# Optimization experiments

Measured on AMD Instinct MI355X. Metric: run time of the kernel, lower is better.

Reference implementation:

```python
import jax, jax.numpy as jnp
import numpy as np

D_MODEL = 192   # embed_dim
DEPTH = 24
D_INNER = 384   # expand=2 * d_model
D_STATE = 16
D_CONV = 4
DT_RANK = 12    # ceil(192/16)
B = 8
IMG = 224
P = 16          # patch size / stride


def setup_inputs() -> dict:
    key = jax.random.key(0)
    ks = jax.random.split(key, 10)
    s = lambda k, shp, sc=0.02: jax.random.normal(k, shp, jnp.float32) * sc
    return {
        "x": jax.random.normal(ks[0], (B, 3, IMG, IMG), jnp.float32),
        "pe_w": s(ks[1], (D_MODEL, 3, P, P)),
        "pe_b": jnp.zeros((D_MODEL,), jnp.float32),
        "norm_w": jnp.ones((DEPTH, D_MODEL), jnp.float32),
        "norm_b": jnp.zeros((DEPTH, D_MODEL), jnp.float32),
        "in_proj_w": s(ks[2], (DEPTH, 2 * D_INNER, D_MODEL)),
        "conv_w": s(ks[3], (DEPTH, D_INNER, D_CONV), 0.1),
        "conv_b": jnp.zeros((DEPTH, D_INNER), jnp.float32),
        "xproj_w": s(ks[4], (DEPTH, DT_RANK + 2 * D_STATE, D_INNER)),
        "dtproj_w": s(ks[5], (DEPTH, D_INNER, DT_RANK), 0.1),
        "dtproj_b": s(ks[6], (DEPTH, D_INNER), 0.1),
        "A_log": jnp.broadcast_to(jnp.log(jnp.arange(1.0, D_STATE + 1.0, dtype=jnp.float32)), (DEPTH, D_INNER, D_STATE)).astype(jnp.float32),
        "D_param": jnp.ones((DEPTH, D_INNER), jnp.float32),
        "outproj_w": s(ks[7], (DEPTH, D_MODEL, D_INNER)),
        "normf_w": jnp.ones((D_MODEL,), jnp.float32),
        "normf_b": jnp.zeros((D_MODEL,), jnp.float32),
    }


def _layernorm(x, w, b, eps=1e-5):
    mu = x.mean(-1, keepdims=True)
    var = ((x - mu) ** 2).mean(-1, keepdims=True)
    return (x - mu) * jax.lax.rsqrt(var + eps) * w + b


def _causal_dwconv(x, w, b):
    # x: [B, L, d_inner]; depthwise causal conv1d (mamba conv1d, padding=d_conv-1, truncated to L)
    xt = jnp.pad(x.swapaxes(1, 2), ((0, 0), (0, 0), (D_CONV - 1, 0)))  # [B, di, L+3]
    y = jax.lax.conv_general_dilated(xt, w[:, None, :], (1,), 'VALID',
                                     feature_group_count=w.shape[0])
    return (y + b[:, None]).swapaxes(1, 2)  # [B, L, di]


def _selective_scan(u, dt, Bm, Cm, A, Dp):
    # u, dt: [B, L, di]; Bm, Cm: [B, L, ds]; A: [di, ds]; Dp: [di]
    dA = jnp.exp(dt[..., None] * A)                         # [B, L, di, ds]
    dBu = (dt * u)[..., None] * Bm[:, :, None, :]           # [B, L, di, ds]

    def step(h, inp):
        dA_t, dBu_t, C_t = inp
        h = dA_t * h + dBu_t                                # [B, di, ds]
        return h, jnp.einsum('bds,bs->bd', h, C_t)

    h0 = jnp.zeros((u.shape[0], A.shape[0], A.shape[1]), u.dtype)
    _, ys = jax.lax.scan(step, h0,
                         (dA.swapaxes(0, 1), dBu.swapaxes(0, 1), Cm.swapaxes(0, 1)))
    return ys.swapaxes(0, 1) + u * Dp                       # [B, L, di]


def _mamba(x, ipw, cw, cb, xpw, dtw, dtb, Alog, Dp, opw):
    xz = jnp.einsum('bld,ed->ble', x, ipw)                  # [B, L, 2*di]
    xin, z = jnp.split(xz, 2, axis=-1)
    xin = jax.nn.silu(_causal_dwconv(xin, cw, cb))
    xdbl = jnp.einsum('bld,ed->ble', xin, xpw)              # [B, L, dt_rank+2*ds]
    dt = jax.nn.softplus(jnp.einsum('blr,dr->bld', xdbl[..., :DT_RANK], dtw) + dtb)
    Bm = xdbl[..., DT_RANK:DT_RANK + D_STATE]
    Cm = xdbl[..., DT_RANK + D_STATE:]
    A = -jnp.exp(Alog)
    y = _selective_scan(xin, dt, Bm, Cm, A, Dp)
    y = y * jax.nn.silu(z)
    return jnp.einsum('bld,ed->ble', y, opw)                # [B, L, D]


def reference(x, pe_w, pe_b, norm_w, norm_b, in_proj_w, conv_w, conv_b,
              xproj_w, dtproj_w, dtproj_b, A_log, D_param, outproj_w,
              normf_w, normf_b):
    # PatchEmbed: conv stride 16 -> flatten -> [B, 196, 192]
    feat = jax.lax.conv_general_dilated(x, pe_w, (P, P), 'VALID') + pe_b[None, :, None, None]
    h = feat.reshape(feat.shape[0], D_MODEL, -1).swapaxes(1, 2)
    residual = None
    for i in range(DEPTH):
        residual = h if residual is None else residual + h
        hn = _layernorm(residual, norm_w[i], norm_b[i])
        h = _mamba(hn, in_proj_w[i], conv_w[i], conv_b[i], xproj_w[i],
                   dtproj_w[i], dtproj_b[i], A_log[i], D_param[i], outproj_w[i])
    residual = residual + h
    return _layernorm(residual, normf_w, normf_b)           # [B, 196, 192]
```

## Files before the change

### kernel.cpp

```cpp
#include <hip/hip_runtime.h>
#include <hip/hip_bf16.h>


#define NTOK   1568
#define DMODEL 192
#define DINNER 384
#define DSTATE 16
#define DTRANK 12
#define DEPTH  24
#define LSEQ   196
#define TCH    49
#define LDA    40

typedef __attribute__((ext_vector_type(8))) short short8;
typedef __attribute__((ext_vector_type(4))) short short4v;
typedef __attribute__((ext_vector_type(4))) float floatx4;

__device__ inline short f2bf(float f) {
    __hip_bfloat16 h = __float2bfloat16(f);
    return *reinterpret_cast<short*>(&h);
}

#define PR1 884736
#define PR2 1327104
#define PR3 1363968
#define PR4 1769472
#define PR5 1880064
#define PR6 3084288
__global__ __launch_bounds__(256) void prep(
    const float* __restrict__ inw, const float* __restrict__ outw,
    const float* __restrict__ pew, const float* __restrict__ xpw,
    const float* __restrict__ dtw, const float* __restrict__ x,
    short* __restrict__ w_in, short* __restrict__ w_out,
    short* __restrict__ w_pe, float* __restrict__ xpwT,
    float* __restrict__ dtwT, __hip_bfloat16* __restrict__ patches)
{
    int idx = blockIdx.x * 256 + threadIdx.x;
    if (idx < PR3) {
        float4 v; short* dst;
        if (idx < PR1)      { v = ((const float4*)inw)[idx];        dst = w_in  + (size_t)idx * 4; }
        else if (idx < PR2) { int i = idx - PR1; v = ((const float4*)outw)[i]; dst = w_out + (size_t)i * 4; }
        else                { int i = idx - PR2; v = ((const float4*)pew)[i];  dst = w_pe  + (size_t)i * 4; }
        short4v o;
        o[0] = f2bf(v.x); o[1] = f2bf(v.y); o[2] = f2bf(v.z); o[3] = f2bf(v.w);
        *(short4v*)dst = o;
    } else if (idx < PR4) {
        int i = idx - PR3;
        int layer = i / 16896, rem = i % 16896;
        int k = rem / 44, e = rem % 44;
        xpwT[i] = xpw[(size_t)layer * 16896 + e * 384 + k];
    } else if (idx < PR5) {
        int i = idx - PR4;
        int layer = i / 4608, rem = i % 4608;
        int r = rem / 384, d = rem % 384;
        dtwT[i] = dtw[(size_t)layer * 4608 + d * 12 + r];
    } else if (idx < PR6) {
        int i = idx - PR5;
        int tok = i / 768, e = i % 768;
        int b = tok / LSEQ, l = tok % LSEQ;
        int py = l / 14, px = l % 14;
        int ic = e >> 8, rem = e & 255, ky = rem >> 4, kx = rem & 15;
        patches[i] = __float2bfloat16(x[((b * 3 + ic) * 224 + py * 16 + ky) * 224 + px * 16 + kx]);
    }
}

template<int K>
__global__ __launch_bounds__(256) void gemm_in(
    const __hip_bfloat16* __restrict__ A, const short* __restrict__ Wb,
    float* __restrict__ C, int M, int N)
{
    __shared__ short As[64 * LDA];
    __shared__ short Ws[64 * LDA];
    int tid = threadIdx.x;
    int m0 = blockIdx.x * 64, n0 = blockIdx.y * 64;
    int wv = tid >> 6, lane = tid & 63;
    int fm = lane & 15, q = lane >> 4;
    int row = tid >> 2, kc = (tid & 3) * 8;
    const short* Ab = (const short*)A;
    floatx4 acc[4];
#pragma unroll
    for (int nt = 0; nt < 4; ++nt) acc[nt] = (floatx4){0.f, 0.f, 0.f, 0.f};

#pragma unroll
    for (int k0 = 0; k0 < K; k0 += 32) {
        {
            int m = m0 + row;
            short8 v = {0,0,0,0,0,0,0,0};
            if (m < M) v = *(const short8*)&Ab[(size_t)m * K + k0 + kc];
            *(short8*)&As[row * LDA + kc] = v;
        }
        {
            short8 w = *(const short8*)&Wb[(size_t)(n0 + row) * K + k0 + kc];
            *(short8*)&Ws[row * LDA + kc] = w;
        }
        __syncthreads();
        short8 af = *(const short8*)&As[(wv * 16 + fm) * LDA + q * 8];
#pragma unroll
        for (int nt = 0; nt < 4; ++nt) {
            short8 bf = *(const short8*)&Ws[(nt * 16 + fm) * LDA + q * 8];
            acc[nt] = __builtin_amdgcn_mfma_f32_16x16x32_bf16(af, bf, acc[nt], 0, 0, 0);
        }
        __syncthreads();
    }
#pragma unroll
    for (int nt = 0; nt < 4; ++nt) {
        int col = n0 + nt * 16 + fm;
#pragma unroll
        for (int r = 0; r < 4; ++r) {
            int mrow = m0 + wv * 16 + q * 4 + r;
            if (mrow < M) C[(size_t)mrow * N + col] = acc[nt][r];
        }
    }
}

template<int K>
__global__ __launch_bounds__(256) void gemm_ln(
    const __hip_bfloat16* __restrict__ A, const short* __restrict__ Wb,
    const float* __restrict__ bias, float* __restrict__ residual,
    __hip_bfloat16* __restrict__ hn, float* __restrict__ outf,
    const float* __restrict__ lnw, const float* __restrict__ lnb,
    int accumulate)
{
    __shared__ short As[16 * LDA];
    __shared__ short Ws[192 * LDA];
    __shared__ float slw[192], slb[192], sbias[192];
    __shared__ float sS1[4][16], sS2[4][16];
    int tid = threadIdx.x;
    int m0 = blockIdx.x * 16;
    int wv = tid >> 6, lane = tid & 63;
    int fm = lane & 15, q = lane >> 4;
    int wrow = tid >> 2, kc = (tid & 3) * 8;
    if (tid < 192) {
        slw[tid] = lnw[tid];
        slb[tid] = lnb[tid];
        sbias[tid] = bias ? bias[tid] : 0.f;
    }
    const short* Ab = (const short*)A;
    floatx4 acc[3];
#pragma unroll
    for (int j = 0; j < 3; ++j) acc[j] = (floatx4){0.f, 0.f, 0.f, 0.f};

    short8 aR = {0,0,0,0,0,0,0,0};
    short8 wR[3];
    if (tid < 64) aR = *(const short8*)&Ab[(size_t)(m0 + (tid >> 2)) * K + kc];
#pragma unroll
    for (int j = 0; j < 3; ++j)
        wR[j] = *(const short8*)&Wb[(size_t)(wrow + 64 * j) * K + kc];

    for (int k0 = 0; k0 < K; k0 += 32) {
        if (tid < 64) *(short8*)&As[(tid >> 2) * LDA + kc] = aR;
#pragma unroll
        for (int j = 0; j < 3; ++j)
            *(short8*)&Ws[(wrow + 64 * j) * LDA + kc] = wR[j];
        __syncthreads();
        int kn = k0 + 32;
        if (kn < K) {
            if (tid < 64) aR = *(const short8*)&Ab[(size_t)(m0 + (tid >> 2)) * K + kn + kc];
#pragma unroll
            for (int j = 0; j < 3; ++j)
                wR[j] = *(const short8*)&Wb[(size_t)(wrow + 64 * j) * K + kn + kc];
        }
        short8 af = *(const short8*)&As[fm * LDA + q * 8];
#pragma unroll
        for (int j = 0; j < 3; ++j) {
            int ct = wv * 3 + j;
            short8 bf = *(const short8*)&Ws[(ct * 16 + fm) * LDA + q * 8];
            acc[j] = __builtin_amdgcn_mfma_f32_16x16x32_bf16(af, bf, acc[j], 0, 0, 0);
        }
        __syncthreads();
    }

    float v[3][4];
#pragma unroll
    for (int r = 0; r < 4; ++r) {
        int m = m0 + q * 4 + r;
#pragma unroll
        for (int j = 0; j < 3; ++j) {
            int col = (wv * 3 + j) * 16 + fm;
            float t = acc[j][r] + sbias[col];
            if (accumulate) t += residual[(size_t)m * DMODEL + col];
            v[j][r] = t;
        }
    }
#pragma unroll
    for (int r = 0; r < 4; ++r) {
        int m = m0 + q * 4 + r;
#pragma unroll
        for (int j = 0; j < 3; ++j)
            residual[(size_t)m * DMODEL + (wv * 3 + j) * 16 + fm] = v[j][r];
    }
#pragma unroll
    for (int r = 0; r < 4; ++r) {
        float s1 = v[0][r] + v[1][r] + v[2][r];
        float s2 = v[0][r]*v[0][r] + v[1][r]*v[1][r] + v[2][r]*v[2][r];
        s1 += __shfl_xor(s1, 1); s2 += __shfl_xor(s2, 1);
        s1 += __shfl_xor(s1, 2); s2 += __shfl_xor(s2, 2);
        s1 += __shfl_xor(s1, 4); s2 += __shfl_xor(s2, 4);
        s1 += __shfl_xor(s1, 8); s2 += __shfl_xor(s2, 8);
        if (fm == 0) { sS1[wv][q * 4 + r] = s1; sS2[wv][q * 4 + r] = s2; }
    }
    __syncthreads();
#pragma unroll
    for (int r = 0; r < 4; ++r) {
        int row = q * 4 + r;
        int m = m0 + row;
        float S1 = sS1[0][row] + sS1[1][row] + sS1[2][row] + sS1[3][row];
        float S2 = sS2[0][row] + sS2[1][row] + sS2[2][row] + sS2[3][row];
        float mean = S1 * (1.f / DMODEL);
        float var  = S2 * (1.f / DMODEL) - mean * mean;
        float rstd = rsqrtf(var + 1e-5f);
#pragma unroll
        for (int j = 0; j < 3; ++j) {
            int col = (wv * 3 + j) * 16 + fm;
            float o = (v[j][r] - mean) * rstd * slw[col] + slb[col];
            if (outf) outf[(size_t)m * DMODEL + col] = o;
            else      hn[(size_t)m * DMODEL + col] = __float2bfloat16(o);
        }
    }
}

__global__ __launch_bounds__(256) void conv_xproj_dt(
    const float* __restrict__ xz, const float* __restrict__ cw,
    const float* __restrict__ cb, const float* __restrict__ xpwT,
    const float* __restrict__ dtwT, const float* __restrict__ dtb,
    float* __restrict__ u, float* __restrict__ dtg, float* __restrict__ bcg)
{
    __shared__ float sxz[7 * 384];
    __shared__ float su[4 * 384];
    __shared__ float sx[4 * 48];
    int blk = blockIdx.x;
    int b = blk / 49, c = blk % 49;
    int l0 = c * 4;
    int tid = threadIdx.x;

    for (int idx = tid; idx < 7 * 384; idx += 256) {
        int t = idx / 384, d = idx % 384;
        int l = l0 - 3 + t;
        sxz[idx] = (l >= 0) ? xz[(size_t)(b * LSEQ + l) * 768 + d] : 0.f;
    }
    __syncthreads();

    for (int idx = tid; idx < 4 * 384; idx += 256) {
        int t = idx / 384, d = idx % 384;
        float4 w4 = *(const float4*)&cw[d * 4];
        float acc = cb[d]
            + sxz[t * 384 + d]       * w4.x
            + sxz[(t + 1) * 384 + d] * w4.y
            + sxz[(t + 2) * 384 + d] * w4.z
            + sxz[(t + 3) * 384 + d] * w4.w;
        float sig = 1.f / (1.f + __expf(-acc));
        float val = acc * sig;
        su[idx] = val;
        u[(size_t)(b * LSEQ + l0 + t) * 384 + d] = val;
    }
    __syncthreads();

    {
        int wv = tid >> 6, e = tid & 63;
        if (e < 44) {
            float a0 = 0.f, a1 = 0.f, a2 = 0.f, a3 = 0.f;
            const float* ur = &su[wv * 384];
            for (int j = 0; j < 384; j += 4) {
                a0 += ur[j]     * xpwT[(j    ) * 44 + e];
                a1 += ur[j + 1] * xpwT[(j + 1) * 44 + e];
                a2 += ur[j + 2] * xpwT[(j + 2) * 44 + e];
                a3 += ur[j + 3] * xpwT[(j + 3) * 44 + e];
            }
            sx[wv * 48 + e] = (a0 + a1) + (a2 + a3);
        }
    }
    __syncthreads();

    for (int idx = tid; idx < 4 * 384; idx += 256) {
        int t = idx / 384, d = idx % 384;
        float acc = dtb[d];
#pragma unroll
        for (int r = 0; r < DTRANK; ++r) acc += sx[t * 48 + r] * dtwT[r * 384 + d];
        float sp = (acc > 20.f) ? acc : log1pf(__expf(acc));
        dtg[(size_t)(b * LSEQ + l0 + t) * 384 + d] = sp;
    }
    if (tid < 128) {
        int t = tid >> 5, j = tid & 31;
        bcg[(size_t)(b * LSEQ + l0 + t) * 32 + j] = sx[t * 48 + 12 + j];
    }
}

#define SPAD 272
__global__ __launch_bounds__(256) void scan_kernel(
    const float* __restrict__ u, const float* __restrict__ dtg,
    const float* __restrict__ bc, const float* __restrict__ xz,
    const float* __restrict__ Alog, const float* __restrict__ Dp,
    __hip_bfloat16* __restrict__ y)
{
    __shared__ float sdt[TCH][16];
    __shared__ float su_[TCH][16];
    __shared__ float sz_[TCH][16];
    __shared__ float sB_[TCH][16];
    __shared__ float sC_[TCH][16];
    __shared__ float sprod[TCH][SPAD];

    int b  = blockIdx.x / 24;
    int dg = blockIdx.x % 24;
    int tid = threadIdx.x;
    int s = tid & 15, dl = tid >> 4;
    int d = dg * 16 + dl;
    float Ads = -expf(Alog[d * DSTATE + s]);
    float Dd2 = Dp[dg * 16 + (tid & 15)];
    float h = 0.f;

    for (int c0 = 0; c0 < LSEQ; c0 += TCH) {
        if (tid < TCH * 4) {
            int t = tid >> 2, j4 = (tid & 3) * 4;
            size_t tok = (size_t)(b * LSEQ + c0 + t);
            *(float4*)&sdt[t][j4] = *(const float4*)&dtg[tok * DINNER + dg * 16 + j4];
            *(float4*)&su_[t][j4] = *(const float4*)&u  [tok * DINNER + dg * 16 + j4];
            *(float4*)&sz_[t][j4] = *(const float4*)&xz [tok * 768 + DINNER + dg * 16 + j4];
            *(float4*)&sB_[t][j4] = *(const float4*)&bc [tok * 32 + j4];
            *(float4*)&sC_[t][j4] = *(const float4*)&bc [tok * 32 + 16 + j4];
        }
        __syncthreads();

#pragma unroll 7
        for (int t = 0; t < TCH; ++t) {
            float dtv = sdt[t][dl];
            float uv  = su_[t][dl];
            float Bv  = sB_[t][s];
            float Cv  = sC_[t][s];
            float dA  = __expf(dtv * Ads);
            h = dA * h + (dtv * uv) * Bv;
            sprod[t][dl * 17 + s] = h * Cv;
        }
        __syncthreads();

        for (int i = tid; i < TCH * 16; i += 256) {
            int t = i >> 4, dl2 = i & 15;
            float sum = 0.f;
#pragma unroll
            for (int j = 0; j < 16; ++j) sum += sprod[t][dl2 * 17 + j];
            float uv = su_[t][dl2];
            float zv = sz_[t][dl2];
            float sig = 1.f / (1.f + __expf(-zv));
            y[(size_t)(b * LSEQ + c0 + t) * DINNER + dg * 16 + dl2] =
                __float2bfloat16((sum + uv * Dd2) * (zv * sig));
        }
        __syncthreads();
    }
}

extern "C" void kernel_launch(void* const* d_in, const int* in_sizes, int n_in,
                              void* d_out, int out_size, void* d_ws, size_t ws_size,
                              hipStream_t stream)
{
    const float* x         = (const float*)d_in[0];
    const float* pe_w      = (const float*)d_in[1];
    const float* pe_b      = (const float*)d_in[2];
    const float* norm_w    = (const float*)d_in[3];
    const float* norm_b    = (const float*)d_in[4];
    const float* in_proj_w = (const float*)d_in[5];
    const float* conv_w    = (const float*)d_in[6];
    const float* conv_b    = (const float*)d_in[7];
    const float* xproj_w   = (const float*)d_in[8];
    const float* dtproj_w  = (const float*)d_in[9];
    const float* dtproj_b  = (const float*)d_in[10];
    const float* A_log     = (const float*)d_in[11];
    const float* D_param   = (const float*)d_in[12];
    const float* outproj_w = (const float*)d_in[13];
    const float* normf_w   = (const float*)d_in[14];
    const float* normf_b   = (const float*)d_in[15];

    float* ws = (float*)d_ws;
    float* residual = ws;
    float* xz       = residual + 301056;
    float* ubuf     = xz + 1204224;
    float* dtbuf    = ubuf + 602112;
    float* bcbuf    = dtbuf + 602112;
    __hip_bfloat16* hn      = (__hip_bfloat16*)(ws + 2759680);
    __hip_bfloat16* ybf     = (__hip_bfloat16*)(ws + 2910208);
    __hip_bfloat16* patches = (__hip_bfloat16*)(ws + 3211264);
    short* w_in  = (short*)(ws + 3813376);
    short* w_out = (short*)(ws + 5582848);
    short* w_pe  = (short*)(ws + 6467584);
    float* xpwT  = ws + 6541312;
    float* dtwT  = xpwT + 405504;

    prep<<<12048, 256, 0, stream>>>(
        in_proj_w, outproj_w, pe_w, xproj_w, dtproj_w, x,
        w_in, w_out, w_pe, xpwT, dtwT, patches);
    gemm_ln<768><<<98, 256, 0, stream>>>(
        patches, w_pe, pe_b, residual, hn, nullptr, norm_w, norm_b, 0);

    for (int i = 0; i < DEPTH; ++i) {
        int last = (i == DEPTH - 1);
        gemm_in<192><<<dim3(25, 12), 256, 0, stream>>>(
            hn, w_in + (size_t)i * 768 * DMODEL, xz, NTOK, 768);
        conv_xproj_dt<<<392, 256, 0, stream>>>(
            xz, conv_w + (size_t)i * DINNER * 4, conv_b + (size_t)i * DINNER,
            xpwT + (size_t)i * 384 * 44, dtwT + (size_t)i * 12 * 384,
            dtproj_b + (size_t)i * DINNER, ubuf, dtbuf, bcbuf);
        scan_kernel<<<192, 256, 0, stream>>>(
            ubuf, dtbuf, bcbuf, xz, A_log + (size_t)i * DINNER * DSTATE,
            D_param + (size_t)i * DINNER, ybf);
        gemm_ln<384><<<98, 256, 0, stream>>>(
            ybf, w_out + (size_t)i * DMODEL * DINNER, nullptr, residual, hn,
            last ? (float*)d_out : nullptr,
            last ? normf_w : norm_w + (i + 1) * DMODEL,
            last ? normf_b : norm_b + (i + 1) * DMODEL,
            1);
    }
}
```

Measured before the change: 1.421 ms.

## Recompute conv and dt projection inside scan; load full K in gemm_in

The conv+xproj kernel now writes only the 44-wide xdbl projection. The scan kernel recomputes the causal depthwise conv, SiLU, dt projection and softplus for its 16-channel slice, which removes the u/dt/bc intermediate buffers and their global round trips. gemm_in is specialised to K=192 and loads the whole K extent into shared memory once, replacing the per-32 chunk loop and its barriers. The cost is redundant conv/SiLU work (done in both kernels) and more shared memory and registers per block.

```diff
diff --git a/kernel.cpp b/kernel.cpp
--- a/kernel.cpp
+++ b/kernel.cpp
@@ -11,6 +11,7 @@
 #define LSEQ   196
 #define TCH    49
 #define LDA    40
+#define LDK    200
 
 typedef __attribute__((ext_vector_type(8))) short short8;
 typedef __attribute__((ext_vector_type(4))) short short4v;
@@ -64,43 +65,40 @@
     }
 }
 
-template<int K>
 __global__ __launch_bounds__(256) void gemm_in(
     const __hip_bfloat16* __restrict__ A, const short* __restrict__ Wb,
     float* __restrict__ C, int M, int N)
 {
-    __shared__ short As[64 * LDA];
-    __shared__ short Ws[64 * LDA];
+    __shared__ short As[64 * LDK];
+    __shared__ short Ws[64 * LDK];
     int tid = threadIdx.x;
     int m0 = blockIdx.x * 64, n0 = blockIdx.y * 64;
     int wv = tid >> 6, lane = tid & 63;
     int fm = lane & 15, q = lane >> 4;
-    int row = tid >> 2, kc = (tid & 3) * 8;
     const short* Ab = (const short*)A;
+
+    for (int i = tid; i < 1536; i += 256) {
+        int row = i / 24, kcc = (i % 24) * 8;
+        int m = m0 + row;
+        short8 v = {0,0,0,0,0,0,0,0};
+        if (m < M) v = *(const short8*)&Ab[(size_t)m * DMODEL + kcc];
+        *(short8*)&As[row * LDK + kcc] = v;
+        short8 w = *(const short8*)&Wb[(size_t)(n0 + row) * DMODEL + kcc];
+        *(short8*)&Ws[row * LDK + kcc] = w;
+    }
+    __syncthreads();
+
     floatx4 acc[4];
 #pragma unroll
     for (int nt = 0; nt < 4; ++nt) acc[nt] = (floatx4){0.f, 0.f, 0.f, 0.f};
-
-#pragma unroll
-    for (int k0 = 0; k0 < K; k0 += 32) {
-        {
-            int m = m0 + row;
-            short8 v = {0,0,0,0,0,0,0,0};
-            if (m < M) v = *(const short8*)&Ab[(size_t)m * K + k0 + kc];
-            *(short8*)&As[row * LDA + kc] = v;
-        }
-        {
-            short8 w = *(const short8*)&Wb[(size_t)(n0 + row) * K + k0 + kc];
-            *(short8*)&Ws[row * LDA + kc] = w;
-        }
-        __syncthreads();
-        short8 af = *(const short8*)&As[(wv * 16 + fm) * LDA + q * 8];
+#pragma unroll
+    for (int k = 0; k < 6; ++k) {
+        short8 af = *(const short8*)&As[(wv * 16 + fm) * LDK + k * 32 + q * 8];
 #pragma unroll
         for (int nt = 0; nt < 4; ++nt) {
-            short8 bf = *(const short8*)&Ws[(nt * 16 + fm) * LDA + q * 8];
+            short8 bf = *(const short8*)&Ws[(nt * 16 + fm) * LDK + k * 32 + q * 8];
             acc[nt] = __builtin_amdgcn_mfma_f32_16x16x32_bf16(af, bf, acc[nt], 0, 0, 0);
         }
-        __syncthreads();
     }
 #pragma unroll
     for (int nt = 0; nt < 4; ++nt) {
@@ -219,15 +217,13 @@
     }
 }
 
-__global__ __launch_bounds__(256) void conv_xproj_dt(
+__global__ __launch_bounds__(256) void conv_xproj(
     const float* __restrict__ xz, const float* __restrict__ cw,
     const float* __restrict__ cb, const float* __restrict__ xpwT,
-    const float* __restrict__ dtwT, const float* __restrict__ dtb,
-    float* __restrict__ u, float* __restrict__ dtg, float* __restrict__ bcg)
+    float* __restrict__ xdbl)
 {
     __shared__ float sxz[7 * 384];
     __shared__ float su[4 * 384];
-    __shared__ float sx[4 * 48];
     int blk = blockIdx.x;
     int b = blk / 49, c = blk % 49;
     int l0 = c * 4;
@@ -249,9 +245,7 @@
             + sxz[(t + 2) * 384 + d] * w4.z
             + sxz[(t + 3) * 384 + d] * w4.w;
         float sig = 1.f / (1.f + __expf(-acc));
-        float val = acc * sig;
-        su[idx] = val;
-        u[(size_t)(b * LSEQ + l0 + t) * 384 + d] = val;
+        su[idx] = acc * sig;
     }
     __syncthreads();
 
@@ -266,32 +260,20 @@
                 a2 += ur[j + 2] * xpwT[(j + 2) * 44 + e];
                 a3 += ur[j + 3] * xpwT[(j + 3) * 44 + e];
             }
-            sx[wv * 48 + e] = (a0 + a1) + (a2 + a3);
-        }
-    }
-    __syncthreads();
-
-    for (int idx = tid; idx < 4 * 384; idx += 256) {
-        int t = idx / 384, d = idx % 384;
-        float acc = dtb[d];
-#pragma unroll
-        for (int r = 0; r < DTRANK; ++r) acc += sx[t * 48 + r] * dtwT[r * 384 + d];
-        float sp = (acc > 20.f) ? acc : log1pf(__expf(acc));
-        dtg[(size_t)(b * LSEQ + l0 + t) * 384 + d] = sp;
-    }
-    if (tid < 128) {
-        int t = tid >> 5, j = tid & 31;
-        bcg[(size_t)(b * LSEQ + l0 + t) * 32 + j] = sx[t * 48 + 12 + j];
+            xdbl[(size_t)(b * LSEQ + l0 + wv) * 44 + e] = (a0 + a1) + (a2 + a3);
+        }
     }
 }
 
 #define SPAD 272
 __global__ __launch_bounds__(256) void scan_kernel(
-    const float* __restrict__ u, const float* __restrict__ dtg,
-    const float* __restrict__ bc, const float* __restrict__ xz,
+    const float* __restrict__ xz, const float* __restrict__ xdbl,
+    const float* __restrict__ cw, const float* __restrict__ cb,
+    const float* __restrict__ dtwT, const float* __restrict__ dtb,
     const float* __restrict__ Alog, const float* __restrict__ Dp,
     __hip_bfloat16* __restrict__ y)
 {
+    __shared__ float sxin[52 * 16];
     __shared__ float sdt[TCH][16];
     __shared__ float su_[TCH][16];
     __shared__ float sz_[TCH][16];
@@ -306,17 +288,66 @@
     int d = dg * 16 + dl;
     float Ads = -expf(Alog[d * DSTATE + s]);
     float Dd2 = Dp[dg * 16 + (tid & 15)];
+
+    int t_ = tid >> 2, j4 = (tid & 3) * 4;
+    float4 wdt[12], dtb4, wc0, wc1, wc2, wc3, cb4;
+    if (tid < 196) {
+        dtb4 = *(const float4*)&dtb[dg * 16 + j4];
+#pragma unroll
+        for (int r = 0; r < 12; ++r)
+            wdt[r] = *(const float4*)&dtwT[r * 384 + dg * 16 + j4];
+        wc0 = *(const float4*)&cw[(dg * 16 + j4 + 0) * 4];
+        wc1 = *(const float4*)&cw[(dg * 16 + j4 + 1) * 4];
+        wc2 = *(const float4*)&cw[(dg * 16 + j4 + 2) * 4];
+        wc3 = *(const float4*)&cw[(dg * 16 + j4 + 3) * 4];
+        cb4 = *(const float4*)&cb[dg * 16 + j4];
+    }
+
     float h = 0.f;
-
     for (int c0 = 0; c0 < LSEQ; c0 += TCH) {
-        if (tid < TCH * 4) {
-            int t = tid >> 2, j4 = (tid & 3) * 4;
+        if (tid < 208) {
+            int tt = tid >> 2, jj = (tid & 3) * 4;
+            int l = c0 - 3 + tt;
+            float4 v = make_float4(0.f, 0.f, 0.f, 0.f);
+            if (l >= 0) v = *(const float4*)&xz[(size_t)(b * LSEQ + l) * 768 + dg * 16 + jj];
+            *(float4*)&sxin[tt * 16 + jj] = v;
+        }
+        __syncthreads();
+
+        if (tid < 196) {
+            int t = t_;
             size_t tok = (size_t)(b * LSEQ + c0 + t);
-            *(float4*)&sdt[t][j4] = *(const float4*)&dtg[tok * DINNER + dg * 16 + j4];
-            *(float4*)&su_[t][j4] = *(const float4*)&u  [tok * DINNER + dg * 16 + j4];
-            *(float4*)&sz_[t][j4] = *(const float4*)&xz [tok * 768 + DINNER + dg * 16 + j4];
-            *(float4*)&sB_[t][j4] = *(const float4*)&bc [tok * 32 + j4];
-            *(float4*)&sC_[t][j4] = *(const float4*)&bc [tok * 32 + 16 + j4];
+            float4 x0 = *(const float4*)&sxin[(t    ) * 16 + j4];
+            float4 x1 = *(const float4*)&sxin[(t + 1) * 16 + j4];
+            float4 x2 = *(const float4*)&sxin[(t + 2) * 16 + j4];
+            float4 x3 = *(const float4*)&sxin[(t + 3) * 16 + j4];
+            float4 uu;
+            uu.x = cb4.x + x0.x * wc0.x + x1.x * wc0.y + x2.x * wc0.z + x3.x * wc0.w;
+            uu.y = cb4.y + x0.y * wc1.x + x1.y * wc1.y + x2.y * wc1.z + x3.y * wc1.w;
+            uu.z = cb4.z + x0.z * wc2.x + x1.z * wc2.y + x2.z * wc2.z + x3.z * wc2.w;
+            uu.w = cb4.w + x0.w * wc3.x + x1.w * wc3.y + x2.w * wc3.z + x3.w * wc3.w;
+            uu.x = uu.x * (1.f / (1.f + __expf(-uu.x)));
+            uu.y = uu.y * (1.f / (1.f + __expf(-uu.y)));
+            uu.z = uu.z * (1.f / (1.f + __expf(-uu.z)));
+            uu.w = uu.w * (1.f / (1.f + __expf(-uu.w)));
+            *(float4*)&su_[t][j4] = uu;
+            float4 xa = *(const float4*)&xdbl[tok * 44 + 0];
+            float4 xb = *(const float4*)&xdbl[tok * 44 + 4];
+            float4 xc = *(const float4*)&xdbl[tok * 44 + 8];
+            float4 a4 = dtb4;
+#define ACCR(X, W) { a4.x += (X) * (W).x; a4.y += (X) * (W).y; a4.z += (X) * (W).z; a4.w += (X) * (W).w; }
+            ACCR(xa.x, wdt[0]) ACCR(xa.y, wdt[1]) ACCR(xa.z, wdt[2])  ACCR(xa.w, wdt[3])
+            ACCR(xb.x, wdt[4]) ACCR(xb.y, wdt[5]) ACCR(xb.z, wdt[6])  ACCR(xb.w, wdt[7])
+            ACCR(xc.x, wdt[8]) ACCR(xc.y, wdt[9]) ACCR(xc.z, wdt[10]) ACCR(xc.w, wdt[11])
+#undef ACCR
+            a4.x = (a4.x > 20.f) ? a4.x : log1pf(__expf(a4.x));
+            a4.y = (a4.y > 20.f) ? a4.y : log1pf(__expf(a4.y));
+            a4.z = (a4.z > 20.f) ? a4.z : log1pf(__expf(a4.z));
+            a4.w = (a4.w > 20.f) ? a4.w : log1pf(__expf(a4.w));
+            *(float4*)&sdt[t][j4] = a4;
+            *(float4*)&sB_[t][j4] = *(const float4*)&xdbl[tok * 44 + 12 + j4];
+            *(float4*)&sC_[t][j4] = *(const float4*)&xdbl[tok * 44 + 28 + j4];
+            *(float4*)&sz_[t][j4] = *(const float4*)&xz[tok * 768 + DINNER + dg * 16 + j4];
         }
         __syncthreads();
 
@@ -370,18 +401,16 @@
 
     float* ws = (float*)d_ws;
     float* residual = ws;
-    float* xz       = residual + 301056;
-    float* ubuf     = xz + 1204224;
-    float* dtbuf    = ubuf + 602112;
-    float* bcbuf    = dtbuf + 602112;
-    __hip_bfloat16* hn      = (__hip_bfloat16*)(ws + 2759680);
-    __hip_bfloat16* ybf     = (__hip_bfloat16*)(ws + 2910208);
-    __hip_bfloat16* patches = (__hip_bfloat16*)(ws + 3211264);
-    short* w_in  = (short*)(ws + 3813376);
-    short* w_out = (short*)(ws + 5582848);
-    short* w_pe  = (short*)(ws + 6467584);
-    float* xpwT  = ws + 6541312;
-    float* dtwT  = xpwT + 405504;
+    float* xz       = ws + 301056;
+    float* xdbl     = ws + 1505280;
+    __hip_bfloat16* hn      = (__hip_bfloat16*)(ws + 1574272);
+    __hip_bfloat16* ybf     = (__hip_bfloat16*)(ws + 1724800);
+    __hip_bfloat16* patches = (__hip_bfloat16*)(ws + 2025856);
+    short* w_in  = (short*)(ws + 2627968);
+    short* w_out = (short*)(ws + 4397440);
+    short* w_pe  = (short*)(ws + 5282176);
+    float* xpwT  = ws + 5355904;
+    float* dtwT  = ws + 5761408;
 
     prep<<<12048, 256, 0, stream>>>(
         in_proj_w, outproj_w, pe_w, xproj_w, dtproj_w, x,
@@ -391,15 +420,15 @@
 
     for (int i = 0; i < DEPTH; ++i) {
         int last = (i == DEPTH - 1);
-        gemm_in<192><<<dim3(25, 12), 256, 0, stream>>>(
+        gemm_in<<<dim3(25, 12), 256, 0, stream>>>(
             hn, w_in + (size_t)i * 768 * DMODEL, xz, NTOK, 768);
-        conv_xproj_dt<<<392, 256, 0, stream>>>(
+        conv_xproj<<<392, 256, 0, stream>>>(
             xz, conv_w + (size_t)i * DINNER * 4, conv_b + (size_t)i * DINNER,
-            xpwT + (size_t)i * 384 * 44, dtwT + (size_t)i * 12 * 384,
-            dtproj_b + (size_t)i * DINNER, ubuf, dtbuf, bcbuf);
+            xpwT + (size_t)i * 384 * 44, xdbl);
         scan_kernel<<<192, 256, 0, stream>>>(
-            ubuf, dtbuf, bcbuf, xz, A_log + (size_t)i * DINNER * DSTATE,
-            D_param + (size_t)i * DINNER, ybf);
+            xz, xdbl, conv_w + (size_t)i * DINNER * 4, conv_b + (size_t)i * DINNER,
+            dtwT + (size_t)i * 12 * 384, dtproj_b + (size_t)i * DINNER,
+            A_log + (size_t)i * DINNER * DSTATE, D_param + (size_t)i * DINNER, ybf);
         gemm_ln<384><<<98, 256, 0, stream>>>(
             ybf, w_out + (size_t)i * DMODEL * DINNER, nullptr, residual, hn,
             last ? (float*)d_out : nullptr,
```

New measurement: 1.493 ms. 5.0% more time.
